# Kernel optimization log

Measured on AMD Instinct MI355X. Metric: run time of the kernel, lower is better.

The kernel has to match this reference:

```python
import jax, jax.numpy as jnp
import numpy as np

H = 128   # hidden_dim
L = 3     # num_layers
N = 50000
E = 800000
EPS = 1e-5


def setup_inputs() -> dict:
    key = jax.random.key(0)
    ks = jax.random.split(key, 16)
    s = 0.02  # param init scale
    return {
        "edge_index_new": jax.random.randint(ks[0], (2, E), 0, N),
        "aligned_features": jax.random.normal(ks[1], (E, 8), jnp.float32),
        "h_nodes_old": jax.random.normal(ks[2], (N, H), jnp.float32),
        "num_nodes": N,
        # node_fusion: Linear(2H -> H)
        "Wf": jax.random.normal(ks[3], (2 * H, H), jnp.float32) * s,
        "bf": jnp.zeros((H,), jnp.float32),
        # edge_to_weight: Linear(8->H), Linear(H->1)
        "We1": jax.random.normal(ks[4], (8, H), jnp.float32) * s,
        "be1": jnp.zeros((H,), jnp.float32),
        "We2": jax.random.normal(ks[5], (H, 1), jnp.float32) * s,
        "be2": jnp.zeros((1,), jnp.float32),
        # GraphConv per layer: lin_rel (W+b), lin_root (W, no bias)
        "Wrel": jax.random.normal(ks[6], (L, H, H), jnp.float32) * s,
        "brel": jnp.zeros((L, H), jnp.float32),
        "Wroot": jax.random.normal(ks[7], (L, H, H), jnp.float32) * s,
        # LayerNorm per layer
        "gamma": jnp.ones((L, H), jnp.float32),
        "beta": jnp.zeros((L, H), jnp.float32),
        # edge_decoder: Linear(2H+8 -> H), Linear(H -> 1)
        "Wd1": jax.random.normal(ks[8], (2 * H + 8, H), jnp.float32) * s,
        "bd1": jnp.zeros((H,), jnp.float32),
        "Wd2": jax.random.normal(ks[9], (H, 1), jnp.float32) * s,
        "bd2": jnp.zeros((1,), jnp.float32),
    }


def _layer_norm(x, g, b):
    mu = jnp.mean(x, axis=-1, keepdims=True)
    var = jnp.mean((x - mu) ** 2, axis=-1, keepdims=True)
    return (x - mu) * jax.lax.rsqrt(var + EPS) * g + b


def reference(edge_index_new, aligned_features, h_nodes_old, num_nodes,
              Wf, bf, We1, be1, We2, be2,
              Wrel, brel, Wroot, gamma, beta,
              Wd1, bd1, Wd2, bd2):
    dt = h_nodes_old.dtype
    hd = Wf.shape[1]
    # node_fusion(cat([ones, h_old])) ; dropout is identity in eval
    x_init = jnp.ones((num_nodes, hd), dtype=dt)
    x = jax.nn.relu(jnp.concatenate([x_init, h_nodes_old], axis=-1) @ Wf + bf)
    # edge_to_weight -> scalar per edge
    ew = jax.nn.sigmoid(jax.nn.relu(aligned_features @ We1 + be1) @ We2 + be2)[:, 0]
    src, dst = edge_index_new[0], edge_index_new[1]
    n_layers = Wrel.shape[0]
    for l in range(n_layers):
        x_res = x
        # GraphConv: sum_{j->i} w_e * x[j], then lin_rel(agg) + lin_root(x)
        msg = ew[:, None] * x[src]                         # [E, H]
        agg = jax.ops.segment_sum(msg, dst, num_segments=num_nodes)
        h = agg @ Wrel[l] + brel[l] + x @ Wroot[l]
        h = jax.nn.relu(_layer_norm(h, gamma[l], beta[l]))
        x = h + x_res
    # edge decoder on gathered node pairs + raw 8-dim features
    edge_repr = jnp.concatenate([x[src], x[dst], aligned_features], axis=-1)
    hmid = jax.nn.relu(edge_repr @ Wd1 + bd1)
    return hmid @ Wd2 + bd2
```

## Files before the change

kernel.cpp:

```cpp
#include <hip/hip_runtime.h>
#include <hip/hip_bf16.h>

#define H 128
#define LN_EPS 1e-5f

typedef __attribute__((ext_vector_type(8))) short bf16x8;
typedef __attribute__((ext_vector_type(4))) float f32x4;

static __device__ __forceinline__ unsigned short f2bf(float f) {
  unsigned u = __float_as_uint(f);
  unsigned r = (u + 0x7fff + ((u >> 16) & 1)) >> 16;
  return (unsigned short)r;
}
static __device__ __forceinline__ float bf2f(unsigned short s) {
  return __uint_as_float(((unsigned)s) << 16);
}


__global__ void zero_int_kernel(int* __restrict__ p, int n) {
  int i = blockIdx.x * blockDim.x + threadIdx.x;
  if (i < n) p[i] = 0;
}

__global__ void prep_cvec_kernel(const float* __restrict__ Wf, const float* __restrict__ bf,
                                 float* __restrict__ cvec) {
  int j = threadIdx.x;
  float s = bf[j];
  for (int r = 0; r < H; ++r) s += Wf[r * H + j];
  cvec[j] = s;
}

__global__ void count_kernel(const int* __restrict__ ei, int E, int* __restrict__ cnt) {
  int e = blockIdx.x * blockDim.x + threadIdx.x;
  if (e < E) atomicAdd(&cnt[ei[E + e]], 1);
}

__global__ __launch_bounds__(1024) void scan_kernel(const int* __restrict__ cnt,
                                                    int* __restrict__ off,
                                                    int* __restrict__ pos, int N) {
  __shared__ int wtot[16];
  __shared__ int wbase[16];
  __shared__ int s_btot;
  __shared__ int s_carry;
  int tid = threadIdx.x, lane = tid & 63, wid = tid >> 6;
  if (tid == 0) s_carry = 0;
  __syncthreads();
  for (int base = 0; base < N; base += 4096) {
    int i0 = base + tid * 4;
    int v[4];
#pragma unroll
    for (int j = 0; j < 4; ++j) v[j] = (i0 + j < N) ? cnt[i0 + j] : 0;
    int s = v[0] + v[1] + v[2] + v[3];
    int incl = s;
#pragma unroll
    for (int o = 1; o < 64; o <<= 1) {
      int t = __shfl_up(incl, o, 64);
      if (lane >= o) incl += t;
    }
    if (lane == 63) wtot[wid] = incl;
    __syncthreads();
    if (tid == 0) {
      int run = 0;
      for (int w = 0; w < 16; ++w) { wbase[w] = run; run += wtot[w]; }
      s_btot = run;
    }
    __syncthreads();
    int e0 = s_carry + wbase[wid] + (incl - s);
#pragma unroll
    for (int j = 0; j < 4; ++j) {
      if (i0 + j < N) { off[i0 + j] = e0; pos[i0 + j] = e0; }
      e0 += v[j];
    }
    __syncthreads();
    if (tid == 0) s_carry += s_btot;
    __syncthreads();
  }
  if (tid == 0) off[N] = s_carry;
}

__global__ void fill_kernel(const int* __restrict__ ei, const float* __restrict__ ew, int E,
                            int* __restrict__ pos, int* __restrict__ csr_src,
                            float* __restrict__ csr_w) {
  int e = blockIdx.x * blockDim.x + threadIdx.x;
  if (e < E) {
    int d = ei[E + e];
    int p = atomicAdd(&pos[d], 1);
    csr_src[p] = ei[e];
    csr_w[p] = ew[e];
  }
}

__global__ __launch_bounds__(256) void cvt_bf16_kernel(const float* __restrict__ in,
                                                       unsigned short* __restrict__ out,
                                                       long n) {
  long i = ((long)blockIdx.x * blockDim.x + threadIdx.x) * 8;
  if (i >= n) return;
  float4 v0 = *(const float4*)&in[i];
  float4 v1 = *(const float4*)&in[i + 4];
  unsigned short t[8];
  t[0] = f2bf(v0.x); t[1] = f2bf(v0.y); t[2] = f2bf(v0.z); t[3] = f2bf(v0.w);
  t[4] = f2bf(v1.x); t[5] = f2bf(v1.y); t[6] = f2bf(v1.z); t[7] = f2bf(v1.w);
  *(uint4*)&out[i] = *(uint4*)t;
}

__global__ __launch_bounds__(256) void pack_w_kernel(const float* __restrict__ Wf,
                                                     const float* __restrict__ Wrel,
                                                     const float* __restrict__ Wroot,
                                                     const float* __restrict__ Wd1,
                                                     unsigned short* __restrict__ wpk) {
  int id = blockIdx.x * blockDim.x + threadIdx.x;
  if (id >= 9 * 2048) return;
  int l = id & 63, nf = (id >> 6) & 7, kk = (id >> 9) & 3, m = id >> 11;
  const float* src;
  if (m == 0) src = Wf + H * H;
  else if (m <= 3) src = Wrel + (size_t)(m - 1) * H * H;
  else if (m <= 6) src = Wroot + (size_t)(m - 4) * H * H;
  else src = Wd1 + (size_t)(m - 7) * H * H;
  int col = nf * 16 + (l & 15);
  int kbase = kk * 32 + (l >> 4) * 8;
  unsigned short t[8];
#pragma unroll
  for (int j = 0; j < 8; ++j) t[j] = f2bf(src[(size_t)(kbase + j) * H + col]);
  *(uint4*)&wpk[(size_t)id * 8] = *(uint4*)t;
}

__global__ __launch_bounds__(256) void edge_weight_v3_kernel(
    const float* __restrict__ af, const float* __restrict__ We1, const float* __restrict__ be1,
    const float* __restrict__ We2, const float* __restrict__ be2, float* __restrict__ ew, int E) {
  int lane = threadIdx.x & 63;
  int sub = lane & 15;
  int grp = lane >> 4;
  float w1[8][8], b1[8], w2[8];
#pragma unroll
  for (int i = 0; i < 8; ++i)
#pragma unroll
    for (int c = 0; c < 8; ++c) w1[i][c] = We1[i * H + sub * 8 + c];
#pragma unroll
  for (int c = 0; c < 8; ++c) { b1[c] = be1[sub * 8 + c]; w2[c] = We2[sub * 8 + c]; }
  float b2 = be2[0];
  int gw = (blockIdx.x * blockDim.x + threadIdx.x) >> 6;
  int nw = (gridDim.x * blockDim.x) >> 6;
  int n4 = (E + 3) >> 2;
  for (int e4 = gw; e4 < n4; e4 += nw) {
    int e = e4 * 4 + grp;
    bool valid = e < E;
    int ee = valid ? e : E - 1;
    float4 a0 = *(const float4*)&af[(size_t)ee * 8];
    float4 a1 = *(const float4*)&af[(size_t)ee * 8 + 4];
    float afv[8] = {a0.x, a0.y, a0.z, a0.w, a1.x, a1.y, a1.z, a1.w};
    float t[8];
#pragma unroll
    for (int c = 0; c < 8; ++c) t[c] = b1[c];
#pragma unroll
    for (int i = 0; i < 8; ++i)
#pragma unroll
      for (int c = 0; c < 8; ++c) t[c] += afv[i] * w1[i][c];
    float p = 0.f;
#pragma unroll
    for (int c = 0; c < 8; ++c) p += fmaxf(t[c], 0.f) * w2[c];
    p += __shfl_xor(p, 1, 64);
    p += __shfl_xor(p, 2, 64);
    p += __shfl_xor(p, 4, 64);
    p += __shfl_xor(p, 8, 64);
    if (valid && sub == 0) {
      float s = p + b2;
      ew[e] = 1.f / (1.f + expf(-s));
    }
  }
}

template <bool DUAL, int OUT_MODE>
__global__ __launch_bounds__(256) void mfma_gemm_kernel(
    const unsigned short* __restrict__ X1, const unsigned short* __restrict__ Wp1,
    const unsigned short* __restrict__ X2, const unsigned short* __restrict__ Wp2,
    const float* __restrict__ bias, void* __restrict__ Yv, int M) {
  int l = threadIdx.x & 63, w = threadIdx.x >> 6;
  int lr = l & 15, lg = l >> 4;
  int m0 = blockIdx.x * 256 + w * 64;
  f32x4 acc[4][8] = {};
  const int nkk = DUAL ? 8 : 4;
  for (int kk = 0; kk < nkk; ++kk) {
    const unsigned short* X = (DUAL && kk >= 4) ? X2 : X1;
    const unsigned short* Wp = (DUAL && kk >= 4) ? Wp2 : Wp1;
    int k4 = kk & 3;
    bf16x8 a[4];
#pragma unroll
    for (int mi = 0; mi < 4; ++mi) {
      int row = m0 + mi * 16 + lr;
      if (row >= M) row = M - 1;
      a[mi] = *(const bf16x8*)&X[(size_t)row * H + k4 * 32 + lg * 8];
    }
#pragma unroll
    for (int nf = 0; nf < 8; ++nf) {
      bf16x8 b = *(const bf16x8*)&Wp[(size_t)(k4 * 8 + nf) * 512 + l * 8];
#pragma unroll
      for (int mi = 0; mi < 4; ++mi)
        acc[mi][nf] = __builtin_amdgcn_mfma_f32_16x16x32_bf16(a[mi], b, acc[mi][nf], 0, 0, 0);
    }
  }
  float bv[8];
#pragma unroll
  for (int nf = 0; nf < 8; ++nf) bv[nf] = bias ? bias[nf * 16 + lr] : 0.f;
#pragma unroll
  for (int mi = 0; mi < 4; ++mi) {
#pragma unroll
    for (int r = 0; r < 4; ++r) {
      int row = m0 + mi * 16 + lg * 4 + r;
      if (row < M) {
#pragma unroll
        for (int nf = 0; nf < 8; ++nf) {
          float v = acc[mi][nf][r] + bv[nf];
          if (OUT_MODE == 1) v = fmaxf(v, 0.f);
          int col = nf * 16 + lr;
          if (OUT_MODE == 0) ((float*)Yv)[(size_t)row * H + col] = v;
          else ((unsigned short*)Yv)[(size_t)row * H + col] = f2bf(v);
        }
      }
    }
  }
}

__global__ __launch_bounds__(256) void gather_agg_bf_kernel(
    const unsigned short* __restrict__ xbf, const int* __restrict__ off,
    const int* __restrict__ csr_src, const float* __restrict__ csr_w,
    unsigned short* __restrict__ aggbf, int N) {
  int gw = (blockIdx.x * blockDim.x + threadIdx.x) >> 6;
  int lane = threadIdx.x & 63;
  int nw = (gridDim.x * blockDim.x) >> 6;
  for (int n = gw; n < N; n += nw) {
    int s0 = off[n], s1 = off[n + 1];
    float ax = 0.f, ay = 0.f;
    int idx = s0;
    for (; idx + 4 <= s1; idx += 4) {
      int src0 = csr_src[idx + 0], src1 = csr_src[idx + 1];
      int src2 = csr_src[idx + 2], src3 = csr_src[idx + 3];
      float w0 = csr_w[idx + 0], w1 = csr_w[idx + 1];
      float w2 = csr_w[idx + 2], w3 = csr_w[idx + 3];
      unsigned v0 = *(const unsigned*)&xbf[(size_t)src0 * H + lane * 2];
      unsigned v1 = *(const unsigned*)&xbf[(size_t)src1 * H + lane * 2];
      unsigned v2 = *(const unsigned*)&xbf[(size_t)src2 * H + lane * 2];
      unsigned v3 = *(const unsigned*)&xbf[(size_t)src3 * H + lane * 2];
      ax += w0 * bf2f((unsigned short)(v0 & 0xffffu));
      ay += w0 * bf2f((unsigned short)(v0 >> 16));
      ax += w1 * bf2f((unsigned short)(v1 & 0xffffu));
      ay += w1 * bf2f((unsigned short)(v1 >> 16));
      ax += w2 * bf2f((unsigned short)(v2 & 0xffffu));
      ay += w2 * bf2f((unsigned short)(v2 >> 16));
      ax += w3 * bf2f((unsigned short)(v3 & 0xffffu));
      ay += w3 * bf2f((unsigned short)(v3 >> 16));
    }
    for (; idx < s1; ++idx) {
      int src = csr_src[idx];
      float w = csr_w[idx];
      unsigned v = *(const unsigned*)&xbf[(size_t)src * H + lane * 2];
      ax += w * bf2f((unsigned short)(v & 0xffffu));
      ay += w * bf2f((unsigned short)(v >> 16));
    }
    unsigned o = (unsigned)f2bf(ax) | ((unsigned)f2bf(ay) << 16);
    *(unsigned*)&aggbf[(size_t)n * H + lane * 2] = o;
  }
}

__global__ __launch_bounds__(256) void ln_relu_res_bf_kernel(
    const float* __restrict__ h, unsigned short* __restrict__ xbf,
    const float* __restrict__ gamma, const float* __restrict__ beta, int N) {
  int gw = (blockIdx.x * blockDim.x + threadIdx.x) >> 6;
  int lane = threadIdx.x & 63;
  int nw = (gridDim.x * blockDim.x) >> 6;
  for (int n = gw; n < N; n += nw) {
    float2 v = *(const float2*)&h[(size_t)n * H + lane * 2];
    float tot = v.x + v.y;
#pragma unroll
    for (int o = 32; o > 0; o >>= 1) tot += __shfl_xor(tot, o, 64);
    float mu = tot * (1.0f / H);
    float d0 = v.x - mu, d1 = v.y - mu;
    float s2 = d0 * d0 + d1 * d1;
#pragma unroll
    for (int o = 32; o > 0; o >>= 1) s2 += __shfl_xor(s2, o, 64);
    float r = rsqrtf(s2 * (1.0f / H) + LN_EPS);
    float2 g = *(const float2*)&gamma[lane * 2];
    float2 b = *(const float2*)&beta[lane * 2];
    unsigned xo = *(const unsigned*)&xbf[(size_t)n * H + lane * 2];
    float o0 = fmaxf(d0 * r * g.x + b.x, 0.f) + bf2f((unsigned short)(xo & 0xffffu));
    float o1 = fmaxf(d1 * r * g.y + b.y, 0.f) + bf2f((unsigned short)(xo >> 16));
    unsigned res = (unsigned)f2bf(o0) | ((unsigned)f2bf(o1) << 16);
    *(unsigned*)&xbf[(size_t)n * H + lane * 2] = res;
  }
}

__global__ __launch_bounds__(256) void edge_out_v3_kernel(
    const int* __restrict__ ei, const float* __restrict__ af,
    const unsigned short* __restrict__ A, const unsigned short* __restrict__ B,
    const float* __restrict__ Wd1c, const float* __restrict__ Wd2,
    const float* __restrict__ bd2, float* __restrict__ out, int E) {
  int lane = threadIdx.x & 63;
  int sub = lane & 15;
  int grp = lane >> 4;
  float wc[8][8], w2[8];
#pragma unroll
  for (int i = 0; i < 8; ++i)
#pragma unroll
    for (int c = 0; c < 8; ++c) wc[i][c] = Wd1c[i * H + sub * 8 + c];
#pragma unroll
  for (int c = 0; c < 8; ++c) w2[c] = Wd2[sub * 8 + c];
  float b2 = bd2[0];
  int gw = (blockIdx.x * blockDim.x + threadIdx.x) >> 6;
  int nw = (gridDim.x * blockDim.x) >> 6;
  int n4 = (E + 3) >> 2;
  for (int e4 = gw; e4 < n4; e4 += nw) {
    int e = e4 * 4 + grp;
    bool valid = e < E;
    int ee = valid ? e : E - 1;
    int s = ei[ee], d = ei[E + ee];
    uint4 va = *(const uint4*)&A[(size_t)s * H + sub * 8];
    uint4 vb = *(const uint4*)&B[(size_t)d * H + sub * 8];
    float4 a0 = *(const float4*)&af[(size_t)ee * 8];
    float4 a1 = *(const float4*)&af[(size_t)ee * 8 + 4];
    float afv[8] = {a0.x, a0.y, a0.z, a0.w, a1.x, a1.y, a1.z, a1.w};
    const unsigned* pa = (const unsigned*)&va;
    const unsigned* pb = (const unsigned*)&vb;
    float t[8];
#pragma unroll
    for (int q = 0; q < 4; ++q) {
      unsigned av = pa[q], bv = pb[q];
      t[q * 2 + 0] = bf2f((unsigned short)(av & 0xffffu)) + bf2f((unsigned short)(bv & 0xffffu));
      t[q * 2 + 1] = bf2f((unsigned short)(av >> 16)) + bf2f((unsigned short)(bv >> 16));
    }
#pragma unroll
    for (int i = 0; i < 8; ++i)
#pragma unroll
      for (int c = 0; c < 8; ++c) t[c] += afv[i] * wc[i][c];
    float p = 0.f;
#pragma unroll
    for (int c = 0; c < 8; ++c) p += fmaxf(t[c], 0.f) * w2[c];
    p += __shfl_xor(p, 1, 64);
    p += __shfl_xor(p, 2, 64);
    p += __shfl_xor(p, 4, 64);
    p += __shfl_xor(p, 8, 64);
    if (valid && sub == 0) out[e] = p + b2;
  }
}

extern "C" void kernel_launch(void* const* d_in, const int* in_sizes, int n_in, void* d_out,
                              int out_size, void* d_ws, size_t ws_size, hipStream_t stream) {
  const int* ei = (const int*)d_in[0];
  const float* af = (const float*)d_in[1];
  const float* h_old = (const float*)d_in[2];
  const float* Wf = (const float*)d_in[4];
  const float* bf = (const float*)d_in[5];
  const float* We1 = (const float*)d_in[6];
  const float* be1 = (const float*)d_in[7];
  const float* We2 = (const float*)d_in[8];
  const float* be2 = (const float*)d_in[9];
  const float* Wrel = (const float*)d_in[10];
  const float* brel = (const float*)d_in[11];
  const float* Wroot = (const float*)d_in[12];
  const float* gamma = (const float*)d_in[13];
  const float* beta = (const float*)d_in[14];
  const float* Wd1 = (const float*)d_in[15];
  const float* bd1 = (const float*)d_in[16];
  const float* Wd2 = (const float*)d_in[17];
  const float* bd2 = (const float*)d_in[18];
  const int N = in_sizes[2] / H;
  const int E = in_sizes[1] / 8;
  float* out = (float*)d_out;

  char* p = (char*)d_ws;
  auto alloc = [&](size_t b) { char* r = p; p += (b + 255) & ~(size_t)255; return r; };
  int* cnt = (int*)alloc((size_t)N * 4);
  int* pos = (int*)alloc((size_t)N * 4);
  int* off = (int*)alloc((size_t)(N + 1) * 4);
  int* csr_src = (int*)alloc((size_t)E * 4);
  float* csr_w = (float*)alloc((size_t)E * 4);
  float* ew = (float*)alloc((size_t)E * 4);
  float* cvec = (float*)alloc(H * 4);
  unsigned short* wpk = (unsigned short*)alloc((size_t)9 * 16384 * 2);
  unsigned short* xbf = (unsigned short*)alloc((size_t)N * H * 2);
  unsigned short* buf1 = (unsigned short*)alloc((size_t)N * H * 2);
  float* hbuf = (float*)alloc((size_t)N * H * 4);

  unsigned short* hbf = buf1;
  unsigned short* aggbf = buf1;
  unsigned short* Abf = (unsigned short*)hbuf;
  unsigned short* Bbf = (unsigned short*)hbuf + (size_t)N * H;

  hipLaunchKernelGGL(zero_int_kernel, dim3((N + 255) / 256), dim3(256), 0, stream, cnt, N);
  hipLaunchKernelGGL(prep_cvec_kernel, dim3(1), dim3(H), 0, stream, Wf, bf, cvec);
  hipLaunchKernelGGL(count_kernel, dim3((E + 255) / 256), dim3(256), 0, stream, ei, E, cnt);
  hipLaunchKernelGGL(scan_kernel, dim3(1), dim3(1024), 0, stream, cnt, off, pos, N);
  hipLaunchKernelGGL(edge_weight_v3_kernel, dim3(4096), dim3(256), 0, stream, af, We1, be1,
                     We2, be2, ew, E);
  hipLaunchKernelGGL(fill_kernel, dim3((E + 255) / 256), dim3(256), 0, stream, ei, ew, E, pos,
                     csr_src, csr_w);
  hipLaunchKernelGGL(cvt_bf16_kernel, dim3(((long)N * H / 8 + 255) / 256), dim3(256), 0, stream,
                     h_old, hbf, (long)N * H);
  hipLaunchKernelGGL(pack_w_kernel, dim3(72), dim3(256), 0, stream, Wf, Wrel, Wroot, Wd1, wpk);

  int gblocks = (N + 255) / 256;
  hipLaunchKernelGGL((mfma_gemm_kernel<false, 1>), dim3(gblocks), dim3(256), 0, stream, hbf,
                     wpk, (const unsigned short*)nullptr, (const unsigned short*)nullptr, cvec,
                     xbf, N);

  for (int l = 0; l < 3; ++l) {
    hipLaunchKernelGGL(gather_agg_bf_kernel, dim3((N + 3) / 4), dim3(256), 0, stream, xbf, off,
                       csr_src, csr_w, aggbf, N);
    hipLaunchKernelGGL((mfma_gemm_kernel<true, 0>), dim3(gblocks), dim3(256), 0, stream, aggbf,
                       wpk + (size_t)(1 + l) * 16384, xbf, wpk + (size_t)(4 + l) * 16384,
                       brel + l * H, hbuf, N);
    hipLaunchKernelGGL(ln_relu_res_bf_kernel, dim3((N + 3) / 4), dim3(256), 0, stream, hbuf,
                       xbf, gamma + l * H, beta + l * H, N);
  }

  hipLaunchKernelGGL((mfma_gemm_kernel<false, 2>), dim3(gblocks), dim3(256), 0, stream, xbf,
                     wpk + (size_t)7 * 16384, (const unsigned short*)nullptr,
                     (const unsigned short*)nullptr, bd1, Abf, N);
  hipLaunchKernelGGL((mfma_gemm_kernel<false, 2>), dim3(gblocks), dim3(256), 0, stream, xbf,
                     wpk + (size_t)8 * 16384, (const unsigned short*)nullptr,
                     (const unsigned short*)nullptr, (const float*)nullptr, Bbf, N);
  hipLaunchKernelGGL(edge_out_v3_kernel, dim3(4096), dim3(256), 0, stream, ei, af, Abf, Bbf,
                     Wd1 + 2 * H * H, Wd2, bd2, out, E);
}
```

Before: 512.8 us.

## Fuse LayerNorm into layer GEMM, merge decoder GEMMs, pack CSR entries

Fuses the fp32-to-bf16 conversion into the initial fusion GEMM and moves LayerNorm, ReLU and the residual into the layer GEMM epilogue, removing the fp32 intermediate buffer and separate LN kernel. The two decoder projections are computed in one kernel sharing the A loads. CSR source and weight are interleaved into one uint2 array, and the gather is unrolled by 8 with masked tails. The GEMM row tile is halved to 128 rows per block, and prep_cvec uses 1024 threads; in-place update of x relies on row-disjoint blocks.

```diff
diff --git a/kernel.cpp b/kernel.cpp
--- a/kernel.cpp
+++ b/kernel.cpp
@@ -22,12 +22,22 @@
   if (i < n) p[i] = 0;
 }
 
-__global__ void prep_cvec_kernel(const float* __restrict__ Wf, const float* __restrict__ bf,
-                                 float* __restrict__ cvec) {
-  int j = threadIdx.x;
-  float s = bf[j];
-  for (int r = 0; r < H; ++r) s += Wf[r * H + j];
-  cvec[j] = s;
+__global__ __launch_bounds__(1024) void prep_cvec_kernel(const float* __restrict__ Wf,
+                                                         const float* __restrict__ bf,
+                                                         float* __restrict__ cvec) {
+  __shared__ float part[8][128];
+  int tid = threadIdx.x;
+  int col = tid & 127, seg = tid >> 7;
+  float s = 0.f;
+  for (int r = seg * 16; r < seg * 16 + 16; ++r) s += Wf[r * H + col];
+  part[seg][col] = s;
+  __syncthreads();
+  if (tid < 128) {
+    float t = bf[tid];
+#pragma unroll
+    for (int g = 0; g < 8; ++g) t += part[g][tid];
+    cvec[tid] = t;
+  }
 }
 
 __global__ void count_kernel(const int* __restrict__ ei, int E, int* __restrict__ cnt) {
@@ -79,28 +89,13 @@
 }
 
 __global__ void fill_kernel(const int* __restrict__ ei, const float* __restrict__ ew, int E,
-                            int* __restrict__ pos, int* __restrict__ csr_src,
-                            float* __restrict__ csr_w) {
+                            int* __restrict__ pos, uint2* __restrict__ csr) {
   int e = blockIdx.x * blockDim.x + threadIdx.x;
   if (e < E) {
     int d = ei[E + e];
     int p = atomicAdd(&pos[d], 1);
-    csr_src[p] = ei[e];
-    csr_w[p] = ew[e];
-  }
-}
-
-__global__ __launch_bounds__(256) void cvt_bf16_kernel(const float* __restrict__ in,
-                                                       unsigned short* __restrict__ out,
-                                                       long n) {
-  long i = ((long)blockIdx.x * blockDim.x + threadIdx.x) * 8;
-  if (i >= n) return;
-  float4 v0 = *(const float4*)&in[i];
-  float4 v1 = *(const float4*)&in[i + 4];
-  unsigned short t[8];
-  t[0] = f2bf(v0.x); t[1] = f2bf(v0.y); t[2] = f2bf(v0.z); t[3] = f2bf(v0.w);
-  t[4] = f2bf(v1.x); t[5] = f2bf(v1.y); t[6] = f2bf(v1.z); t[7] = f2bf(v1.w);
-  *(uint4*)&out[i] = *(uint4*)t;
+    csr[p] = make_uint2((unsigned)ei[e], __float_as_uint(ew[e]));
+  }
 }
 
 __global__ __launch_bounds__(256) void pack_w_kernel(const float* __restrict__ Wf,
@@ -169,122 +164,196 @@
   }
 }
 
-template <bool DUAL, int OUT_MODE>
-__global__ __launch_bounds__(256) void mfma_gemm_kernel(
-    const unsigned short* __restrict__ X1, const unsigned short* __restrict__ Wp1,
-    const unsigned short* __restrict__ X2, const unsigned short* __restrict__ Wp2,
-    const float* __restrict__ bias, void* __restrict__ Yv, int M) {
+__global__ __launch_bounds__(256) void gemm_init_kernel(
+    const float* __restrict__ Xf, const unsigned short* __restrict__ Wp,
+    const float* __restrict__ bias, unsigned short* __restrict__ Y, int M) {
   int l = threadIdx.x & 63, w = threadIdx.x >> 6;
   int lr = l & 15, lg = l >> 4;
-  int m0 = blockIdx.x * 256 + w * 64;
-  f32x4 acc[4][8] = {};
-  const int nkk = DUAL ? 8 : 4;
-  for (int kk = 0; kk < nkk; ++kk) {
-    const unsigned short* X = (DUAL && kk >= 4) ? X2 : X1;
-    const unsigned short* Wp = (DUAL && kk >= 4) ? Wp2 : Wp1;
-    int k4 = kk & 3;
-    bf16x8 a[4];
-#pragma unroll
-    for (int mi = 0; mi < 4; ++mi) {
+  int m0 = blockIdx.x * 128 + w * 32;
+  f32x4 acc[2][8] = {};
+  for (int kk = 0; kk < 4; ++kk) {
+    bf16x8 a[2];
+#pragma unroll
+    for (int mi = 0; mi < 2; ++mi) {
       int row = m0 + mi * 16 + lr;
       if (row >= M) row = M - 1;
-      a[mi] = *(const bf16x8*)&X[(size_t)row * H + k4 * 32 + lg * 8];
+      const float* xp = &Xf[(size_t)row * H + kk * 32 + lg * 8];
+      float4 u0 = *(const float4*)xp;
+      float4 u1 = *(const float4*)(xp + 4);
+      unsigned short t[8] = {f2bf(u0.x), f2bf(u0.y), f2bf(u0.z), f2bf(u0.w),
+                             f2bf(u1.x), f2bf(u1.y), f2bf(u1.z), f2bf(u1.w)};
+      a[mi] = *(const bf16x8*)t;
     }
 #pragma unroll
     for (int nf = 0; nf < 8; ++nf) {
-      bf16x8 b = *(const bf16x8*)&Wp[(size_t)(k4 * 8 + nf) * 512 + l * 8];
-#pragma unroll
-      for (int mi = 0; mi < 4; ++mi)
+      bf16x8 b = *(const bf16x8*)&Wp[(size_t)(kk * 8 + nf) * 512 + l * 8];
+#pragma unroll
+      for (int mi = 0; mi < 2; ++mi)
         acc[mi][nf] = __builtin_amdgcn_mfma_f32_16x16x32_bf16(a[mi], b, acc[mi][nf], 0, 0, 0);
     }
   }
   float bv[8];
 #pragma unroll
-  for (int nf = 0; nf < 8; ++nf) bv[nf] = bias ? bias[nf * 16 + lr] : 0.f;
-#pragma unroll
-  for (int mi = 0; mi < 4; ++mi) {
+  for (int nf = 0; nf < 8; ++nf) bv[nf] = bias[nf * 16 + lr];
+#pragma unroll
+  for (int mi = 0; mi < 2; ++mi)
 #pragma unroll
     for (int r = 0; r < 4; ++r) {
       int row = m0 + mi * 16 + lg * 4 + r;
       if (row < M) {
 #pragma unroll
+        for (int nf = 0; nf < 8; ++nf)
+          Y[(size_t)row * H + nf * 16 + lr] = f2bf(fmaxf(acc[mi][nf][r] + bv[nf], 0.f));
+      }
+    }
+}
+
+__global__ __launch_bounds__(256) void gemm_layer_ln_kernel(
+    const unsigned short* __restrict__ Agg, const unsigned short* __restrict__ WpRel,
+    unsigned short* __restrict__ Xio, const unsigned short* __restrict__ WpRoot,
+    const float* __restrict__ brel, const float* __restrict__ gamma,
+    const float* __restrict__ beta, int M) {
+  int l = threadIdx.x & 63, w = threadIdx.x >> 6;
+  int lr = l & 15, lg = l >> 4;
+  int m0 = blockIdx.x * 128 + w * 32;
+  f32x4 acc[2][8] = {};
+  for (int kk = 0; kk < 8; ++kk) {
+    const unsigned short* X = (kk >= 4) ? Xio : Agg;
+    const unsigned short* Wp = (kk >= 4) ? WpRoot : WpRel;
+    int k4 = kk & 3;
+    bf16x8 a[2] = {};
+#pragma unroll
+    for (int mi = 0; mi < 2; ++mi) {
+      int row = m0 + mi * 16 + lr;
+      if (row < M) a[mi] = *(const bf16x8*)&X[(size_t)row * H + k4 * 32 + lg * 8];
+    }
+#pragma unroll
+    for (int nf = 0; nf < 8; ++nf) {
+      bf16x8 b = *(const bf16x8*)&Wp[(size_t)(k4 * 8 + nf) * 512 + l * 8];
+#pragma unroll
+      for (int mi = 0; mi < 2; ++mi)
+        acc[mi][nf] = __builtin_amdgcn_mfma_f32_16x16x32_bf16(a[mi], b, acc[mi][nf], 0, 0, 0);
+    }
+  }
+  float bv[8], gv[8], bev[8];
+#pragma unroll
+  for (int nf = 0; nf < 8; ++nf) {
+    int col = nf * 16 + lr;
+    bv[nf] = brel[col]; gv[nf] = gamma[col]; bev[nf] = beta[col];
+  }
+#pragma unroll
+  for (int mi = 0; mi < 2; ++mi) {
+#pragma unroll
+    for (int r = 0; r < 4; ++r) {
+      int row = m0 + mi * 16 + lg * 4 + r;
+      float hv[8], s1 = 0.f;
+#pragma unroll
+      for (int nf = 0; nf < 8; ++nf) { hv[nf] = acc[mi][nf][r] + bv[nf]; s1 += hv[nf]; }
+      s1 += __shfl_xor(s1, 1, 64);
+      s1 += __shfl_xor(s1, 2, 64);
+      s1 += __shfl_xor(s1, 4, 64);
+      s1 += __shfl_xor(s1, 8, 64);
+      float mu = s1 * (1.0f / H);
+      float s2 = 0.f;
+#pragma unroll
+      for (int nf = 0; nf < 8; ++nf) { float d = hv[nf] - mu; s2 += d * d; }
+      s2 += __shfl_xor(s2, 1, 64);
+      s2 += __shfl_xor(s2, 2, 64);
+      s2 += __shfl_xor(s2, 4, 64);
+      s2 += __shfl_xor(s2, 8, 64);
+      float rstd = rsqrtf(s2 * (1.0f / H) + LN_EPS);
+      if (row < M) {
+#pragma unroll
         for (int nf = 0; nf < 8; ++nf) {
-          float v = acc[mi][nf][r] + bv[nf];
-          if (OUT_MODE == 1) v = fmaxf(v, 0.f);
           int col = nf * 16 + lr;
-          if (OUT_MODE == 0) ((float*)Yv)[(size_t)row * H + col] = v;
-          else ((unsigned short*)Yv)[(size_t)row * H + col] = f2bf(v);
+          float v = fmaxf((hv[nf] - mu) * rstd * gv[nf] + bev[nf], 0.f);
+          v += bf2f(Xio[(size_t)row * H + col]);
+          Xio[(size_t)row * H + col] = f2bf(v);
         }
       }
     }
   }
 }
 
-__global__ __launch_bounds__(256) void gather_agg_bf_kernel(
+__global__ __launch_bounds__(256) void gemm_dec_kernel(
+    const unsigned short* __restrict__ X, const unsigned short* __restrict__ WpA,
+    const unsigned short* __restrict__ WpB, const float* __restrict__ bd1,
+    unsigned short* __restrict__ Aout, unsigned short* __restrict__ Bout, int M) {
+  int l = threadIdx.x & 63, w = threadIdx.x >> 6;
+  int lr = l & 15, lg = l >> 4;
+  int m0 = blockIdx.x * 128 + w * 32;
+  f32x4 accA[2][8] = {};
+  f32x4 accB[2][8] = {};
+  for (int kk = 0; kk < 4; ++kk) {
+    bf16x8 a[2];
+#pragma unroll
+    for (int mi = 0; mi < 2; ++mi) {
+      int row = m0 + mi * 16 + lr;
+      if (row >= M) row = M - 1;
+      a[mi] = *(const bf16x8*)&X[(size_t)row * H + kk * 32 + lg * 8];
+    }
+#pragma unroll
+    for (int nf = 0; nf < 8; ++nf) {
+      bf16x8 bA = *(const bf16x8*)&WpA[(size_t)(kk * 8 + nf) * 512 + l * 8];
+      bf16x8 bB = *(const bf16x8*)&WpB[(size_t)(kk * 8 + nf) * 512 + l * 8];
+#pragma unroll
+      for (int mi = 0; mi < 2; ++mi) {
+        accA[mi][nf] = __builtin_amdgcn_mfma_f32_16x16x32_bf16(a[mi], bA, accA[mi][nf], 0, 0, 0);
+        accB[mi][nf] = __builtin_amdgcn_mfma_f32_16x16x32_bf16(a[mi], bB, accB[mi][nf], 0, 0, 0);
+      }
+    }
+  }
+  float bdv[8];
+#pragma unroll
+  for (int nf = 0; nf < 8; ++nf) bdv[nf] = bd1[nf * 16 + lr];
+#pragma unroll
+  for (int mi = 0; mi < 2; ++mi)
+#pragma unroll
+    for (int r = 0; r < 4; ++r) {
+      int row = m0 + mi * 16 + lg * 4 + r;
+      if (row < M) {
+#pragma unroll
+        for (int nf = 0; nf < 8; ++nf) {
+          int col = nf * 16 + lr;
+          Aout[(size_t)row * H + col] = f2bf(accA[mi][nf][r] + bdv[nf]);
+          Bout[(size_t)row * H + col] = f2bf(accB[mi][nf][r]);
+        }
+      }
+    }
+}
+
+__global__ __launch_bounds__(256) void gather_agg_v2_kernel(
     const unsigned short* __restrict__ xbf, const int* __restrict__ off,
-    const int* __restrict__ csr_src, const float* __restrict__ csr_w,
-    unsigned short* __restrict__ aggbf, int N) {
+    const uint2* __restrict__ csr, unsigned short* __restrict__ aggbf, int N) {
   int gw = (blockIdx.x * blockDim.x + threadIdx.x) >> 6;
   int lane = threadIdx.x & 63;
   int nw = (gridDim.x * blockDim.x) >> 6;
   for (int n = gw; n < N; n += nw) {
     int s0 = off[n], s1 = off[n + 1];
     float ax = 0.f, ay = 0.f;
-    int idx = s0;
-    for (; idx + 4 <= s1; idx += 4) {
-      int src0 = csr_src[idx + 0], src1 = csr_src[idx + 1];
-      int src2 = csr_src[idx + 2], src3 = csr_src[idx + 3];
-      float w0 = csr_w[idx + 0], w1 = csr_w[idx + 1];
-      float w2 = csr_w[idx + 2], w3 = csr_w[idx + 3];
-      unsigned v0 = *(const unsigned*)&xbf[(size_t)src0 * H + lane * 2];
-      unsigned v1 = *(const unsigned*)&xbf[(size_t)src1 * H + lane * 2];
-      unsigned v2 = *(const unsigned*)&xbf[(size_t)src2 * H + lane * 2];
-      unsigned v3 = *(const unsigned*)&xbf[(size_t)src3 * H + lane * 2];
-      ax += w0 * bf2f((unsigned short)(v0 & 0xffffu));
-      ay += w0 * bf2f((unsigned short)(v0 >> 16));
-      ax += w1 * bf2f((unsigned short)(v1 & 0xffffu));
-      ay += w1 * bf2f((unsigned short)(v1 >> 16));
-      ax += w2 * bf2f((unsigned short)(v2 & 0xffffu));
-      ay += w2 * bf2f((unsigned short)(v2 >> 16));
-      ax += w3 * bf2f((unsigned short)(v3 & 0xffffu));
-      ay += w3 * bf2f((unsigned short)(v3 >> 16));
-    }
-    for (; idx < s1; ++idx) {
-      int src = csr_src[idx];
-      float w = csr_w[idx];
-      unsigned v = *(const unsigned*)&xbf[(size_t)src * H + lane * 2];
-      ax += w * bf2f((unsigned short)(v & 0xffffu));
-      ay += w * bf2f((unsigned short)(v >> 16));
+    for (int base = s0; base < s1; base += 8) {
+      unsigned srcv[8];
+      float wv[8];
+#pragma unroll
+      for (int j = 0; j < 8; ++j) {
+        int id = base + j;
+        int cid = id < s1 ? id : s1 - 1;
+        uint2 c = csr[cid];
+        srcv[j] = c.x;
+        wv[j] = (id < s1) ? __uint_as_float(c.y) : 0.f;
+      }
+      unsigned vv[8];
+#pragma unroll
+      for (int j = 0; j < 8; ++j)
+        vv[j] = *(const unsigned*)&xbf[(size_t)srcv[j] * H + lane * 2];
+#pragma unroll
+      for (int j = 0; j < 8; ++j) {
+        ax += wv[j] * bf2f((unsigned short)(vv[j] & 0xffffu));
+        ay += wv[j] * bf2f((unsigned short)(vv[j] >> 16));
+      }
     }
     unsigned o = (unsigned)f2bf(ax) | ((unsigned)f2bf(ay) << 16);
     *(unsigned*)&aggbf[(size_t)n * H + lane * 2] = o;
-  }
-}
-
-__global__ __launch_bounds__(256) void ln_relu_res_bf_kernel(
-    const float* __restrict__ h, unsigned short* __restrict__ xbf,
-    const float* __restrict__ gamma, const float* __restrict__ beta, int N) {
-  int gw = (blockIdx.x * blockDim.x + threadIdx.x) >> 6;
-  int lane = threadIdx.x & 63;
-  int nw = (gridDim.x * blockDim.x) >> 6;
-  for (int n = gw; n < N; n += nw) {
-    float2 v = *(const float2*)&h[(size_t)n * H + lane * 2];
-    float tot = v.x + v.y;
-#pragma unroll
-    for (int o = 32; o > 0; o >>= 1) tot += __shfl_xor(tot, o, 64);
-    float mu = tot * (1.0f / H);
-    float d0 = v.x - mu, d1 = v.y - mu;
-    float s2 = d0 * d0 + d1 * d1;
-#pragma unroll
-    for (int o = 32; o > 0; o >>= 1) s2 += __shfl_xor(s2, o, 64);
-    float r = rsqrtf(s2 * (1.0f / H) + LN_EPS);
-    float2 g = *(const float2*)&gamma[lane * 2];
-    float2 b = *(const float2*)&beta[lane * 2];
-    unsigned xo = *(const unsigned*)&xbf[(size_t)n * H + lane * 2];
-    float o0 = fmaxf(d0 * r * g.x + b.x, 0.f) + bf2f((unsigned short)(xo & 0xffffu));
-    float o1 = fmaxf(d1 * r * g.y + b.y, 0.f) + bf2f((unsigned short)(xo >> 16));
-    unsigned res = (unsigned)f2bf(o0) | ((unsigned)f2bf(o1) << 16);
-    *(unsigned*)&xbf[(size_t)n * H + lane * 2] = res;
   }
 }
 
@@ -370,53 +439,41 @@
   int* cnt = (int*)alloc((size_t)N * 4);
   int* pos = (int*)alloc((size_t)N * 4);
   int* off = (int*)alloc((size_t)(N + 1) * 4);
-  int* csr_src = (int*)alloc((size_t)E * 4);
-  float* csr_w = (float*)alloc((size_t)E * 4);
+  uint2* csr = (uint2*)alloc((size_t)E * 8);
   float* ew = (float*)alloc((size_t)E * 4);
   float* cvec = (float*)alloc(H * 4);
   unsigned short* wpk = (unsigned short*)alloc((size_t)9 * 16384 * 2);
   unsigned short* xbf = (unsigned short*)alloc((size_t)N * H * 2);
-  unsigned short* buf1 = (unsigned short*)alloc((size_t)N * H * 2);
-  float* hbuf = (float*)alloc((size_t)N * H * 4);
-
-  unsigned short* hbf = buf1;
-  unsigned short* aggbf = buf1;
-  unsigned short* Abf = (unsigned short*)hbuf;
-  unsigned short* Bbf = (unsigned short*)hbuf + (size_t)N * H;
+  unsigned short* aggbf = (unsigned short*)alloc((size_t)N * H * 2);
+  unsigned short* buf2 = (unsigned short*)alloc((size_t)N * H * 2);
+
+  unsigned short* Abf = aggbf;
+  unsigned short* Bbf = buf2;
 
   hipLaunchKernelGGL(zero_int_kernel, dim3((N + 255) / 256), dim3(256), 0, stream, cnt, N);
-  hipLaunchKernelGGL(prep_cvec_kernel, dim3(1), dim3(H), 0, stream, Wf, bf, cvec);
+  hipLaunchKernelGGL(prep_cvec_kernel, dim3(1), dim3(1024), 0, stream, Wf, bf, cvec);
   hipLaunchKernelGGL(count_kernel, dim3((E + 255) / 256), dim3(256), 0, stream, ei, E, cnt);
   hipLaunchKernelGGL(scan_kernel, dim3(1), dim3(1024), 0, stream, cnt, off, pos, N);
   hipLaunchKernelGGL(edge_weight_v3_kernel, dim3(4096), dim3(256), 0, stream, af, We1, be1,
                      We2, be2, ew, E);
   hipLaunchKernelGGL(fill_kernel, dim3((E + 255) / 256), dim3(256), 0, stream, ei, ew, E, pos,
-                     csr_src, csr_w);
-  hipLaunchKernelGGL(cvt_bf16_kernel, dim3(((long)N * H / 8 + 255) / 256), dim3(256), 0, stream,
-                     h_old, hbf, (long)N * H);
+                     csr);
   hipLaunchKernelGGL(pack_w_kernel, dim3(72), dim3(256), 0, stream, Wf, Wrel, Wroot, Wd1, wpk);
 
-  int gblocks = (N + 255) / 256;
-  hipLaunchKernelGGL((mfma_gemm_kernel<false, 1>), dim3(gblocks), dim3(256), 0, stream, hbf,
-                     wpk, (const unsigned short*)nullptr, (const unsigned short*)nullptr, cvec,
+  int gblocks = (N + 127) / 128;
+  hipLaunchKernelGGL(gemm_init_kernel, dim3(gblocks), dim3(256), 0, stream, h_old, wpk, cvec,
                      xbf, N);
 
   for (int l = 0; l < 3; ++l) {
-    hipLaunchKernelGGL(gather_agg_bf_kernel, dim3((N + 3) / 4), dim3(256), 0, stream, xbf, off,
-                       csr_src, csr_w, aggbf, N);
-    hipLaunchKernelGGL((mfma_gemm_kernel<true, 0>), dim3(gblocks), dim3(256), 0, stream, aggbf,
+    hipLaunchKernelGGL(gather_agg_v2_kernel, dim3((N + 3) / 4), dim3(256), 0, stream, xbf, off,
+                       csr, aggbf, N);
+    hipLaunchKernelGGL(gemm_layer_ln_kernel, dim3(gblocks), dim3(256), 0, stream, aggbf,
                        wpk + (size_t)(1 + l) * 16384, xbf, wpk + (size_t)(4 + l) * 16384,
-                       brel + l * H, hbuf, N);
-    hipLaunchKernelGGL(ln_relu_res_bf_kernel, dim3((N + 3) / 4), dim3(256), 0, stream, hbuf,
-                       xbf, gamma + l * H, beta + l * H, N);
-  }
-
-  hipLaunchKernelGGL((mfma_gemm_kernel<false, 2>), dim3(gblocks), dim3(256), 0, stream, xbf,
-                     wpk + (size_t)7 * 16384, (const unsigned short*)nullptr,
-                     (const unsigned short*)nullptr, bd1, Abf, N);
-  hipLaunchKernelGGL((mfma_gemm_kernel<false, 2>), dim3(gblocks), dim3(256), 0, stream, xbf,
-                     wpk + (size_t)8 * 16384, (const unsigned short*)nullptr,
-                     (const unsigned short*)nullptr, (const float*)nullptr, Bbf, N);
+                       brel + l * H, gamma + l * H, beta + l * H, N);
+  }
+
+  hipLaunchKernelGGL(gemm_dec_kernel, dim3(gblocks), dim3(256), 0, stream, xbf,
+                     wpk + (size_t)7 * 16384, wpk + (size_t)8 * 16384, bd1, Abf, Bbf, N);
   hipLaunchKernelGGL(edge_out_v3_kernel, dim3(4096), dim3(256), 0, stream, ei, af, Abf, Bbf,
                      Wd1 + 2 * H * H, Wd2, bd2, out, E);
 }
```

New measurement: 466.1 us. -9.1%, faster.
